# Kernel optimization log

Hardware: AMD Instinct MI355X
Metric: run time of the kernel (lower is better)

The kernel has to match this reference:

```python
import jax, jax.numpy as jnp
import numpy as np


def setup_inputs() -> dict:
    key = jax.random.key(0)
    k1, k2, k3, k4, k5 = jax.random.split(key, 5)
    b, n, L, D, m = 8, 8192, 512, 128, 16
    x = jax.random.normal(k1, (b, n, L), dtype=jnp.float32)
    # attention MLP: Linear(L->D, no bias), Tanh, Linear(D->1, no bias)
    W1 = jax.random.normal(k2, (L, D), dtype=jnp.float32) / np.sqrt(L).astype(np.float32)
    W2 = jax.random.normal(k3, (D, 1), dtype=jnp.float32) / np.sqrt(D).astype(np.float32)
    batched_image_ids = jax.random.randint(k4, (b, n), 0, m)  # which image each packed token belongs to
    key_pad_mask = jax.random.bernoulli(k5, 0.1, (b, n))      # True = padding token
    return {"x": x, "W1": W1, "W2": W2,
            "batched_image_ids": batched_image_ids,
            "key_pad_mask": key_pad_mask,
            "max_queries": 16}


def reference(x, W1, W2, batched_image_ids, key_pad_mask, max_queries):
    # Attention scores per token: tanh(x W1) W2 -> [b, n, 1]
    A = jnp.tanh(x @ W1) @ W2
    A = jnp.swapaxes(A, -1, -2)  # [b, 1, n]
    b, n, d = x.shape
    # Per-image pooling mask: token j contributes to query i iff its image id == i and not padded
    image_id_arange = jnp.arange(max_queries)                                    # [m]
    attn_pool_mask = (image_id_arange[None, :, None] == batched_image_ids[:, None, :])
    attn_pool_mask = attn_pool_mask & (~key_pad_mask)[:, None, :]                # [b, m, n]
    neg = -jnp.finfo(A.dtype).max
    A = jnp.where(attn_pool_mask, jnp.broadcast_to(A, (b, max_queries, n)), neg)
    A = jax.nn.softmax(A, axis=-1)                                               # [b, m, n]
    out = jnp.einsum('bmn,bnd->bmd', A, x)                                       # pooled per image
    # num_images == max_queries for every bag -> is_images selects everything
    out = out.reshape(b * max_queries, d)
    return out
```

## Files before the change

kernel.cpp:

```cpp
#include <hip/hip_runtime.h>
#include <hip/hip_bf16.h>
#include <cstdint>
#include <cstddef>

typedef __attribute__((ext_vector_type(8))) short bf16x8;
typedef __attribute__((ext_vector_type(4))) float f32x4;

#define BATCH 8
#define NTOK 8192
#define LDIM 512
#define DDIM 128
#define NQ 16
#define NSEG 8
#define SEGLEN (NTOK / NSEG)

static __device__ __forceinline__ short f2bf(float f) {
  uint32_t u = __float_as_uint(f);
  uint32_t r = u + 0x7fffu + ((u >> 16) & 1u);
  return (short)(r >> 16);
}

static __device__ __forceinline__ bf16x8 cvt8(float4 a, float4 b) {
  union { uint32_t u[4]; bf16x8 v; } r;
  asm("v_cvt_pk_bf16_f32 %0, %1, %2" : "=v"(r.u[0]) : "v"(a.x), "v"(a.y));
  asm("v_cvt_pk_bf16_f32 %0, %1, %2" : "=v"(r.u[1]) : "v"(a.z), "v"(a.w));
  asm("v_cvt_pk_bf16_f32 %0, %1, %2" : "=v"(r.u[2]) : "v"(b.x), "v"(b.y));
  asm("v_cvt_pk_bf16_f32 %0, %1, %2" : "=v"(r.u[3]) : "v"(b.z), "v"(b.w));
  return r.v;
}

static __device__ __forceinline__ bool is_pad(const void* pad, int byteFlag, int j) {
  return byteFlag ? (((const unsigned char*)pad)[j] != 0)
                  : (((const int*)pad)[j] != 0);
}

__global__ __launch_bounds__(256) void k0_wfrag(const float* __restrict__ W1,
                                                short* __restrict__ wfrag,
                                                const unsigned int* __restrict__ pad_raw,
                                                int* __restrict__ flag) {
  int tid = blockIdx.x * blockDim.x + threadIdx.x;
  if (tid < 16 * 8 * 64) {
    int l = tid & 63;
    int t = (tid >> 6) & 7;
    int c = tid >> 9;
    int kbase = c * 32 + (l >> 4) * 8;
    int col = t * 16 + (l & 15);
    bf16x8 frag;
#pragma unroll
    for (int i = 0; i < 8; ++i) frag[i] = f2bf(W1[(size_t)(kbase + i) * DDIM + col]);
    ((bf16x8*)wfrag)[tid] = frag;
  }
  if (blockIdx.x == 0) {
    int any_gt1 = 0;
    for (int i = threadIdx.x; i < 16384; i += 256)
      if (pad_raw[i] > 1u) any_gt1 = 1;
    unsigned long long m = __ballot(any_gt1);
    __shared__ int s[4];
    if ((threadIdx.x & 63) == 0) s[threadIdx.x >> 6] = (m != 0ull) ? 1 : 0;
    __syncthreads();
    if (threadIdx.x == 0) flag[0] = (s[0] | s[1] | s[2] | s[3]);
  }
}

__global__ __launch_bounds__(512, 4) void k1_scores(const float* __restrict__ x,
                                                    const short* __restrict__ wfrag,
                                                    const float* __restrict__ W2,
                                                    float* __restrict__ expw) {
  __shared__ short ldsw[16384];
  const int tid = threadIdx.x, wave = tid >> 6, lane = tid & 63;
  const int rowBase = blockIdx.x * 128 + wave * 16;
  const float* xp = x + (size_t)(rowBase + (lane & 15)) * LDIM + ((lane >> 4) * 8);

#define STAGE(qd)                                                                             \
  {                                                                                           \
    const unsigned int* src_ = (const unsigned int*)wfrag + (qd) * 8192;                      \
    _Pragma("unroll")                                                                         \
    for (int i = 0; i < 4; ++i) {                                                             \
      __builtin_amdgcn_global_load_lds(                                                       \
          (const __attribute__((address_space(1))) unsigned int*)(src_ + (i * 512 + tid) * 4),\
          (__attribute__((address_space(3))) unsigned int*)&ldsw[(i * 512 + wave * 64) * 8],  \
          16, 0, 0);                                                                          \
    }                                                                                         \
  }

#define ALOAD(dst, c)                                  \
  {                                                    \
    dst[0] = *(const float4*)(xp + (c) * 32);          \
    dst[1] = *(const float4*)(xp + (c) * 32 + 4);      \
  }

  f32x4 acc[8];
#pragma unroll
  for (int t = 0; t < 8; ++t) acc[t] = (f32x4){0.f, 0.f, 0.f, 0.f};
  float4 avbuf[6][2];

  STAGE(0);
  ALOAD(avbuf[0], 0);
  ALOAD(avbuf[1], 1);
  ALOAD(avbuf[2], 2);
  ALOAD(avbuf[3], 3);
  ALOAD(avbuf[4], 4);
  ALOAD(avbuf[5], 5);
  __syncthreads();

#pragma unroll
  for (int qd = 0; qd < 4; ++qd) {
#pragma unroll
    for (int cc = 0; cc < 4; ++cc) {
      const int c = qd * 4 + cc;
      bf16x8 af = cvt8(avbuf[c % 6][0], avbuf[c % 6][1]);
      if (c < 10) ALOAD(avbuf[c % 6], c + 6);
#pragma unroll
      for (int t = 0; t < 8; ++t) {
        bf16x8 bfr = *(const bf16x8*)&ldsw[((cc * 8 + t) * 64 + lane) * 8];
        acc[t] = __builtin_amdgcn_mfma_f32_16x16x32_bf16(af, bfr, acc[t], 0, 0, 0);
      }
    }
    if (qd < 3) {
      __syncthreads();
      STAGE(qd + 1);
      __syncthreads();
    }
  }
#undef STAGE
#undef ALOAD

  float w2v[8];
#pragma unroll
  for (int t = 0; t < 8; ++t) w2v[t] = W2[t * 16 + (lane & 15)];
  float asum[4] = {0.f, 0.f, 0.f, 0.f};
#pragma unroll
  for (int t = 0; t < 8; ++t) {
#pragma unroll
    for (int r = 0; r < 4; ++r) {
      float h = 1.f - 2.f / (__expf(2.f * acc[t][r]) + 1.f);
      asum[r] += h * w2v[t];
    }
  }
#pragma unroll
  for (int m = 1; m < 16; m <<= 1) {
#pragma unroll
    for (int r = 0; r < 4; ++r) asum[r] += __shfl_xor(asum[r], m, 64);
  }
  if ((lane & 15) == 0) {
    int rb = rowBase + (lane >> 4) * 4;
#pragma unroll
    for (int r = 0; r < 4; ++r) expw[rb + r] = __expf(asum[r]);
  }
}

__global__ __launch_bounds__(512) void k3_pool(const float* __restrict__ x,
                                               const float* __restrict__ expw,
                                               const int* __restrict__ ids,
                                               const void* __restrict__ pad,
                                               const int* __restrict__ flag,
                                               float* __restrict__ partial,
                                               float* __restrict__ wsum) {
  int blk = blockIdx.x;
  int s = blk & 7, q = (blk >> 3) & 15, b = blk >> 7;
  int wave = threadIdx.x >> 6, lane = threadIdx.x & 63;
  int bfl = flag[0];
  __shared__ float w_u[1024];
  __shared__ unsigned short j_u[1024];
  __shared__ int cnt[8];
  __shared__ float wred[8];

  const int base = b * NTOK;
  const int tokBase = s * SEGLEN + wave * 128;

  int j0 = tokBase + lane, j1 = tokBase + 64 + lane;
  bool mem0 = (ids[base + j0] == q) && !is_pad(pad, bfl, base + j0);
  bool mem1 = (ids[base + j1] == q) && !is_pad(pad, bfl, base + j1);
  float wt0 = mem0 ? expw[base + j0] : 0.f;
  float wt1 = mem1 ? expw[base + j1] : 0.f;
  unsigned long long m0 = __ballot(mem0), m1 = __ballot(mem1);
  int c0w = __popcll(m0), c1w = __popcll(m1);
  if (lane == 0) cnt[wave] = c0w + c1w;
  __syncthreads();

  int wpos = 0;
#pragma unroll
  for (int w = 0; w < 8; ++w) if (w < wave) wpos += cnt[w];
  const int total = cnt[0] + cnt[1] + cnt[2] + cnt[3] + cnt[4] + cnt[5] + cnt[6] + cnt[7];

  unsigned long long below = (1ull << lane) - 1ull;
  if (mem0) {
    int pos = wpos + __popcll(m0 & below);
    w_u[pos] = wt0; j_u[pos] = (unsigned short)j0;
  }
  if (mem1) {
    int pos = wpos + c0w + __popcll(m1 & below);
    w_u[pos] = wt1; j_u[pos] = (unsigned short)j1;
  }
  float wacc = wt0 + wt1;
#pragma unroll
  for (int m = 1; m < 64; m <<= 1) wacc += __shfl_xor(wacc, m, 64);
  if (lane == 0) wred[wave] = wacc;
  __syncthreads();

  int grp = threadIdx.x >> 7, ct = threadIdx.x & 127;
  int c0 = ct * 4;
  int per = (total + 3) >> 2;
  int e0 = grp * per;
  int e1 = e0 + per; if (e1 > total) e1 = total;
  float4 av = {0.f, 0.f, 0.f, 0.f};
  if (e0 < e1) {
    float4 cur = *(const float4*)(x + (size_t)(base + j_u[e0]) * LDIM + c0);
    int e = e0;
    for (; e + 1 < e1; ++e) {
      float4 nxt = *(const float4*)(x + (size_t)(base + j_u[e + 1]) * LDIM + c0);
      float wt = w_u[e];
      av.x = fmaf(wt, cur.x, av.x); av.y = fmaf(wt, cur.y, av.y);
      av.z = fmaf(wt, cur.z, av.z); av.w = fmaf(wt, cur.w, av.w);
      cur = nxt;
    }
    float wt = w_u[e];
    av.x = fmaf(wt, cur.x, av.x); av.y = fmaf(wt, cur.y, av.y);
    av.z = fmaf(wt, cur.z, av.z); av.w = fmaf(wt, cur.w, av.w);
  }
  *(float4*)(partial + ((size_t)(blk * 4 + grp)) * LDIM + c0) = av;
  if (threadIdx.x == 0)
    wsum[blk] = wred[0] + wred[1] + wred[2] + wred[3] + wred[4] + wred[5] + wred[6] + wred[7];
}

__global__ __launch_bounds__(512) void k4_reduce(const float* __restrict__ partial,
                                                 const float* __restrict__ wsum,
                                                 float* __restrict__ out) {
  int bq = blockIdx.x;
  int b = bq >> 4, q = bq & 15;
  int c = threadIdx.x;
  float ws = 0.f;
#pragma unroll
  for (int s = 0; s < 8; ++s) ws += wsum[b * 128 + q * 8 + s];
  float ps = 0.f;
#pragma unroll
  for (int s = 0; s < 8; ++s)
#pragma unroll
    for (int g = 0; g < 4; ++g)
      ps += partial[((size_t)((b * 128 + q * 8 + s) * 4 + g)) * LDIM + c];
  out[bq * 512 + c] = (ws > 0.f) ? (ps / ws) : 0.f;
}

extern "C" void kernel_launch(void* const* d_in, const int* in_sizes, int n_in,
                              void* d_out, int out_size, void* d_ws, size_t ws_size,
                              hipStream_t stream) {
  const float* x = (const float*)d_in[0];
  const float* W1 = (const float*)d_in[1];
  const float* W2 = (const float*)d_in[2];
  const int* ids = (const int*)d_in[3];
  const void* pad = d_in[4];
  float* out = (float*)d_out;

  char* ws = (char*)d_ws;
  short* wfrag = (short*)ws;
  int* flag = (int*)(ws + 131072);
  float* expw = (float*)(ws + 131200);
  float* wsum = (float*)(ws + 393344);
  float* partial = (float*)(ws + 397440);

  hipLaunchKernelGGL(k0_wfrag, dim3(32), dim3(256), 0, stream,
                     W1, wfrag, (const unsigned int*)pad, flag);
  hipLaunchKernelGGL(k1_scores, dim3((BATCH * NTOK) / 128), dim3(512), 0, stream,
                     x, wfrag, W2, expw);
  hipLaunchKernelGGL(k3_pool, dim3(BATCH * NQ * NSEG), dim3(512), 0, stream,
                     x, expw, ids, pad, flag, partial, wsum);
  hipLaunchKernelGGL(k4_reduce, dim3(BATCH * NQ), dim3(512), 0, stream,
                     partial, wsum, out);
}
```

Before: 67.25 us.

## Stage x tiles through swizzled LDS with double-buffered async W1/x loads in scorer

The score kernel now uses 256-thread blocks handling 64 rows each. The x tiles are staged into LDS with global_load_lds using an XOR swizzle, and both the W1 fragments and the x chunks are double-buffered, so the next chunk loads while the current one runs on MFMA. This replaces direct register prefetch of x and the paired barriers around each W1 stage. It uses 80KB of LDS per block, which lowers occupancy, and it issues a barrier on every chunk.

Measured after the change: 69.00 us. 1.03x slower.

```diff
diff --git a/kernel.cpp b/kernel.cpp
--- a/kernel.cpp
+++ b/kernel.cpp
@@ -62,68 +62,73 @@
   }
 }
 
-__global__ __launch_bounds__(512, 4) void k1_scores(const float* __restrict__ x,
+__global__ __launch_bounds__(256, 2) void k1_scores(const float* __restrict__ x,
                                                     const short* __restrict__ wfrag,
                                                     const float* __restrict__ W2,
                                                     float* __restrict__ expw) {
-  __shared__ short ldsw[16384];
+  __shared__ __align__(16) char smem[81920];
+  short* ldsw = (short*)smem;
+  char* xchunk = smem + 65536;
   const int tid = threadIdx.x, wave = tid >> 6, lane = tid & 63;
-  const int rowBase = blockIdx.x * 128 + wave * 16;
-  const float* xp = x + (size_t)(rowBase + (lane & 15)) * LDIM + ((lane >> 4) * 8);
-
-#define STAGE(qd)                                                                             \
-  {                                                                                           \
-    const unsigned int* src_ = (const unsigned int*)wfrag + (qd) * 8192;                      \
-    _Pragma("unroll")                                                                         \
-    for (int i = 0; i < 4; ++i) {                                                             \
-      __builtin_amdgcn_global_load_lds(                                                       \
-          (const __attribute__((address_space(1))) unsigned int*)(src_ + (i * 512 + tid) * 4),\
-          (__attribute__((address_space(3))) unsigned int*)&ldsw[(i * 512 + wave * 64) * 8],  \
-          16, 0, 0);                                                                          \
-    }                                                                                         \
-  }
-
-#define ALOAD(dst, c)                                  \
-  {                                                    \
-    dst[0] = *(const float4*)(xp + (c) * 32);          \
-    dst[1] = *(const float4*)(xp + (c) * 32 + 4);      \
+  const int g = lane >> 4;
+  const int rl = (wave << 4) + (lane & 15);
+  const int rowB = blockIdx.x * 64;
+
+#define STAGE_W(qd, wb)                                                                     \
+  {                                                                                         \
+    const unsigned int* srcw_ = (const unsigned int*)wfrag + (qd) * 8192;                   \
+    _Pragma("unroll")                                                                       \
+    for (int i = 0; i < 8; ++i) {                                                           \
+      int off_ = (i * 4 + wave) * 64 + lane;                                                \
+      __builtin_amdgcn_global_load_lds(                                                     \
+          (const __attribute__((address_space(1))) unsigned int*)(srcw_ + off_ * 4),        \
+          (__attribute__((address_space(3))) unsigned int*)&ldsw[(wb) * 16384 + off_ * 8],  \
+          16, 0, 0);                                                                        \
+    }                                                                                       \
+  }
+
+#define STAGE_X(c, xb)                                                                      \
+  {                                                                                         \
+    _Pragma("unroll")                                                                       \
+    for (int k = 0; k < 2; ++k) {                                                           \
+      int o_ = (wave << 11) + (k << 10) + (lane << 4);          \
+      int lo_ = o_ ^ (((o_ >> 7) & 7) << 4);                 \
+      int r_ = lo_ >> 7, cb_ = lo_ & 127;                                                   \
+      const char* srcx_ =                                                                   \
+          (const char*)x + ((size_t)(rowB + r_) * LDIM + (size_t)(c) * 32) * 4 + cb_;       \
+      __builtin_amdgcn_global_load_lds(                                                     \
+          (const __attribute__((address_space(1))) unsigned int*)srcx_,                     \
+          (__attribute__((address_space(3))) unsigned int*)(xchunk + (xb) * 8192 + o_),     \
+          16, 0, 0);                                                                        \
+    }                                                                                       \
   }
 
   f32x4 acc[8];
 #pragma unroll
   for (int t = 0; t < 8; ++t) acc[t] = (f32x4){0.f, 0.f, 0.f, 0.f};
-  float4 avbuf[6][2];
-
-  STAGE(0);
-  ALOAD(avbuf[0], 0);
-  ALOAD(avbuf[1], 1);
-  ALOAD(avbuf[2], 2);
-  ALOAD(avbuf[3], 3);
-  ALOAD(avbuf[4], 4);
-  ALOAD(avbuf[5], 5);
+
+  STAGE_W(0, 0);
+  STAGE_X(0, 0);
   __syncthreads();
 
-#pragma unroll
-  for (int qd = 0; qd < 4; ++qd) {
-#pragma unroll
-    for (int cc = 0; cc < 4; ++cc) {
-      const int c = qd * 4 + cc;
-      bf16x8 af = cvt8(avbuf[c % 6][0], avbuf[c % 6][1]);
-      if (c < 10) ALOAD(avbuf[c % 6], c + 6);
-#pragma unroll
-      for (int t = 0; t < 8; ++t) {
-        bf16x8 bfr = *(const bf16x8*)&ldsw[((cc * 8 + t) * 64 + lane) * 8];
-        acc[t] = __builtin_amdgcn_mfma_f32_16x16x32_bf16(af, bfr, acc[t], 0, 0, 0);
-      }
+  const int sw = (rl & 7) << 4;
+  const int xrbase = rl * 128 + g * 32;
+
+  for (int c = 0; c < 16; ++c) {
+    if ((c & 3) == 0 && c < 12) STAGE_W((c >> 2) + 1, ((c >> 2) + 1) & 1);
+    if (c < 15) STAGE_X(c + 1, (c + 1) & 1);
+    const char* xc = xchunk + (c & 1) * 8192;
+    float4 a0 = *(const float4*)(xc + (xrbase ^ sw));
+    float4 a1 = *(const float4*)(xc + ((xrbase + 16) ^ sw));
+    bf16x8 af = cvt8(a0, a1);
+    const int wq = (c >> 2) & 1, cc = c & 3;
+#pragma unroll
+    for (int t = 0; t < 8; ++t) {
+      bf16x8 bfr = *(const bf16x8*)&ldsw[wq * 16384 + ((cc * 8 + t) * 64 + lane) * 8];
+      acc[t] = __builtin_amdgcn_mfma_f32_16x16x32_bf16(af, bfr, acc[t], 0, 0, 0);
     }
-    if (qd < 3) {
-      __syncthreads();
-      STAGE(qd + 1);
-      __syncthreads();
-    }
-  }
-#undef STAGE
-#undef ALOAD
+    if (c < 15) __syncthreads();
+  }
 
   float w2v[8];
 #pragma unroll
@@ -143,7 +148,7 @@
     for (int r = 0; r < 4; ++r) asum[r] += __shfl_xor(asum[r], m, 64);
   }
   if ((lane & 15) == 0) {
-    int rb = rowBase + (lane >> 4) * 4;
+    int rb = rowB + wave * 16 + (lane >> 4) * 4;
 #pragma unroll
     for (int r = 0; r < 4; ++r) expw[rb + r] = __expf(asum[r]);
   }
@@ -260,7 +265,7 @@
 
   hipLaunchKernelGGL(k0_wfrag, dim3(32), dim3(256), 0, stream,
                      W1, wfrag, (const unsigned int*)pad, flag);
-  hipLaunchKernelGGL(k1_scores, dim3((BATCH * NTOK) / 128), dim3(512), 0, stream,
+  hipLaunchKernelGGL(k1_scores, dim3((BATCH * NTOK) / 64), dim3(256), 0, stream,
                      x, wfrag, W2, expw);
   hipLaunchKernelGGL(k3_pool, dim3(BATCH * NQ * NSEG), dim3(512), 0, stream,
                      x, expw, ids, pad, flag, partial, wsum);
```

## Split score GEMM hidden dimension across wave pairs, halve rows per block

Applied to the files above, without the earlier changes.

Each block in the score kernel now handles 64 rows instead of 128. Pairs of waves split the 128 hidden columns into two halves of 64, and the two partial tanh·W2 sums are combined through shared memory before the exponential. This doubles the grid and halves the accumulator and prefetch registers per wave, aiming at more parallelism and occupancy. In exchange each block stages the full W1 fragment set for half as many rows, which doubles W1 staging traffic, and adds two barriers plus an LDS reduction.

Measured after the change: 76.84 us. +14.2%, slower.

```diff
diff --git a/kernel.cpp b/kernel.cpp
--- a/kernel.cpp
+++ b/kernel.cpp
@@ -67,9 +67,13 @@
                                                     const float* __restrict__ W2,
                                                     float* __restrict__ expw) {
   __shared__ short ldsw[16384];
+  __shared__ float sc[2][64];
   const int tid = threadIdx.x, wave = tid >> 6, lane = tid & 63;
-  const int rowBase = blockIdx.x * 128 + wave * 16;
-  const float* xp = x + (size_t)(rowBase + (lane & 15)) * LDIM + ((lane >> 4) * 8);
+  const int wt = wave & 3;
+  const int th = wave >> 2;
+  const int g = lane >> 4;
+  const int rowB = blockIdx.x * 64;
+  const float* xp = x + (size_t)(rowB + wt * 16 + (lane & 15)) * LDIM + (g * 8);
 
 #define STAGE(qd)                                                                             \
   {                                                                                           \
@@ -89,18 +93,16 @@
     dst[1] = *(const float4*)(xp + (c) * 32 + 4);      \
   }
 
-  f32x4 acc[8];
-#pragma unroll
-  for (int t = 0; t < 8; ++t) acc[t] = (f32x4){0.f, 0.f, 0.f, 0.f};
-  float4 avbuf[6][2];
+  f32x4 acc[4];
+#pragma unroll
+  for (int t = 0; t < 4; ++t) acc[t] = (f32x4){0.f, 0.f, 0.f, 0.f};
+  float4 avbuf[4][2];
 
   STAGE(0);
   ALOAD(avbuf[0], 0);
   ALOAD(avbuf[1], 1);
   ALOAD(avbuf[2], 2);
   ALOAD(avbuf[3], 3);
-  ALOAD(avbuf[4], 4);
-  ALOAD(avbuf[5], 5);
   __syncthreads();
 
 #pragma unroll
@@ -108,12 +110,12 @@
 #pragma unroll
     for (int cc = 0; cc < 4; ++cc) {
       const int c = qd * 4 + cc;
-      bf16x8 af = cvt8(avbuf[c % 6][0], avbuf[c % 6][1]);
-      if (c < 10) ALOAD(avbuf[c % 6], c + 6);
-#pragma unroll
-      for (int t = 0; t < 8; ++t) {
-        bf16x8 bfr = *(const bf16x8*)&ldsw[((cc * 8 + t) * 64 + lane) * 8];
-        acc[t] = __builtin_amdgcn_mfma_f32_16x16x32_bf16(af, bfr, acc[t], 0, 0, 0);
+      bf16x8 af = cvt8(avbuf[c & 3][0], avbuf[c & 3][1]);
+      if (c < 12) ALOAD(avbuf[c & 3], c + 4);
+#pragma unroll
+      for (int tl = 0; tl < 4; ++tl) {
+        bf16x8 bfr = *(const bf16x8*)&ldsw[((cc * 8 + th * 4 + tl) * 64 + lane) * 8];
+        acc[tl] = __builtin_amdgcn_mfma_f32_16x16x32_bf16(af, bfr, acc[tl], 0, 0, 0);
       }
     }
     if (qd < 3) {
@@ -125,16 +127,16 @@
 #undef STAGE
 #undef ALOAD
 
-  float w2v[8];
-#pragma unroll
-  for (int t = 0; t < 8; ++t) w2v[t] = W2[t * 16 + (lane & 15)];
+  float w2v[4];
+#pragma unroll
+  for (int tl = 0; tl < 4; ++tl) w2v[tl] = W2[(th * 4 + tl) * 16 + (lane & 15)];
   float asum[4] = {0.f, 0.f, 0.f, 0.f};
 #pragma unroll
-  for (int t = 0; t < 8; ++t) {
+  for (int tl = 0; tl < 4; ++tl) {
 #pragma unroll
     for (int r = 0; r < 4; ++r) {
-      float h = 1.f - 2.f / (__expf(2.f * acc[t][r]) + 1.f);
-      asum[r] += h * w2v[t];
+      float h = 1.f - 2.f / (__expf(2.f * acc[tl][r]) + 1.f);
+      asum[r] += h * w2v[tl];
     }
   }
 #pragma unroll
@@ -142,11 +144,13 @@
 #pragma unroll
     for (int r = 0; r < 4; ++r) asum[r] += __shfl_xor(asum[r], m, 64);
   }
+  __syncthreads();
   if ((lane & 15) == 0) {
-    int rb = rowBase + (lane >> 4) * 4;
-#pragma unroll
-    for (int r = 0; r < 4; ++r) expw[rb + r] = __expf(asum[r]);
-  }
+#pragma unroll
+    for (int r = 0; r < 4; ++r) sc[th][wt * 16 + g * 4 + r] = asum[r];
+  }
+  __syncthreads();
+  if (tid < 64) expw[rowB + tid] = __expf(sc[0][tid] + sc[1][tid]);
 }
 
 __global__ __launch_bounds__(512) void k3_pool(const float* __restrict__ x,
@@ -260,7 +264,7 @@
 
   hipLaunchKernelGGL(k0_wfrag, dim3(32), dim3(256), 0, stream,
                      W1, wfrag, (const unsigned int*)pad, flag);
-  hipLaunchKernelGGL(k1_scores, dim3((BATCH * NTOK) / 128), dim3(512), 0, stream,
+  hipLaunchKernelGGL(k1_scores, dim3((BATCH * NTOK) / 64), dim3(512), 0, stream,
                      x, wfrag, W2, expw);
   hipLaunchKernelGGL(k3_pool, dim3(BATCH * NQ * NSEG), dim3(512), 0, stream,
                      x, expw, ids, pad, flag, partial, wsum);
```
